# Kernel optimization log

Measured on AMD Instinct MI355X. Metric: run time of the kernel, lower is better.

Reference implementation:

```python
import jax, jax.numpy as jnp
import numpy as np

N_NODES = 100000
N_EDGES = 2000000
D_IN = 4
HID = 64


def setup_inputs() -> dict:
    key = jax.random.key(0)
    ks = jax.random.split(key, 8)
    node_feats = jax.random.normal(ks[0], (N_NODES, D_IN), dtype=jnp.float32)
    pairs = jax.random.randint(ks[1], (N_EDGES, 2), 0, N_NODES, dtype=jnp.int64)
    # Kaiming-ish init scaling
    W1 = jax.random.normal(ks[2], (D_IN, HID), dtype=jnp.float32) / np.sqrt(D_IN)
    b1 = jnp.zeros((HID,), dtype=jnp.float32)
    W2 = jax.random.normal(ks[3], (HID, HID), dtype=jnp.float32) / np.sqrt(HID)
    b2 = jnp.zeros((HID,), dtype=jnp.float32)
    We1 = jax.random.normal(ks[4], (3 * HID, HID), dtype=jnp.float32) / np.sqrt(3 * HID)
    be1 = jnp.zeros((HID,), dtype=jnp.float32)
    We2 = jax.random.normal(ks[5], (HID, 1), dtype=jnp.float32) / np.sqrt(HID)
    be2 = jnp.zeros((1,), dtype=jnp.float32)
    return {"node_feats": node_feats, "pairs": pairs, "W1": W1, "b1": b1,
            "W2": W2, "b2": b2, "We1": We1, "be1": be1, "We2": We2, "be2": be2}


def reference(node_feats, pairs, W1, b1, W2, b2, We1, be1, We2, be2):
    # node MLP: Linear -> ReLU -> Linear -> ReLU
    H = jax.nn.relu(node_feats @ W1 + b1)      # [N, HID]
    H = jax.nn.relu(H @ W2 + b2)               # [N, HID]
    # vectorized gather over all edge pairs (replaces Python loop)
    hu = H[pairs[:, 0]]                        # [E, HID]
    hv = H[pairs[:, 1]]                        # [E, HID]
    E = jnp.concatenate([hu, hv, jnp.abs(hu - hv)], axis=-1)  # [E, 3*HID]
    # edge MLP: Linear -> ReLU -> Linear, squeeze last dim
    scores = (jax.nn.relu(E @ We1 + be1) @ We2 + be2)[:, 0]   # [E]
    return scores
```

## Files before the change

kernel.cpp:

```cpp
#include <hip/hip_runtime.h>

#define N_NODES 100000
#define N_EDGES 2000000

typedef __bf16 bf16x8 __attribute__((ext_vector_type(8)));
typedef float f32x4 __attribute__((ext_vector_type(4)));
typedef float f32x16 __attribute__((ext_vector_type(16)));

#define AS1 __attribute__((address_space(1)))
#define AS3 __attribute__((address_space(3)))

__device__ __forceinline__ unsigned f2bf_rne(float f) {
  unsigned u = __builtin_bit_cast(unsigned, f);
  u += 0x7FFFu + ((u >> 16) & 1u);
  return u >> 16;
}

__device__ __forceinline__ unsigned pack_rhu(float lo, float hi) {
  unsigned ulo = __builtin_bit_cast(unsigned, lo) + 0x8000u;
  unsigned uhi = __builtin_bit_cast(unsigned, hi) + 0x8000u;
  return __builtin_amdgcn_perm(uhi, ulo, 0x07060302u);
}

__device__ __forceinline__ unsigned absdiff_pack(unsigned a, unsigned b) {
  float alo = __builtin_bit_cast(float, a << 16);
  float ahi = __builtin_bit_cast(float, a & 0xFFFF0000u);
  float blo = __builtin_bit_cast(float, b << 16);
  float bhi = __builtin_bit_cast(float, b & 0xFFFF0000u);
  return pack_rhu(fabsf(alo - blo), fabsf(ahi - bhi));
}

__global__ __launch_bounds__(64, 1) void node_mfma_kernel(
    const float* __restrict__ X, const float* __restrict__ W1,
    const float* __restrict__ b1, const float* __restrict__ W2,
    const float* __restrict__ b2, unsigned short* __restrict__ H) {
  const int lane = threadIdx.x;
  const int l15 = lane & 15;
  const int quad = lane >> 4;

  float w1v[2][4][8], b1v[2][8];
#pragma unroll
  for (int c = 0; c < 2; ++c)
#pragma unroll
    for (int j = 0; j < 8; ++j) {
      int col = c * 32 + quad * 8 + j;
      b1v[c][j] = b1[col];
#pragma unroll
      for (int d = 0; d < 4; ++d) w1v[c][d][j] = W1[d * 64 + col];
    }

  uint4 afr[2][4];
#pragma unroll
  for (int c = 0; c < 2; ++c)
#pragma unroll
    for (int mt = 0; mt < 4; ++mt) {
      unsigned w[4];
#pragma unroll
      for (int p = 0; p < 4; ++p) {
        int k = c * 32 + quad * 8 + 2 * p;
        unsigned lo = f2bf_rne(W2[k * 64 + mt * 16 + l15]);
        unsigned hi = f2bf_rne(W2[(k + 1) * 64 + mt * 16 + l15]);
        w[p] = lo | (hi << 16);
      }
      afr[c][mt] = make_uint4(w[0], w[1], w[2], w[3]);
    }
  float b2v[16];
#pragma unroll
  for (int mt = 0; mt < 4; ++mt)
#pragma unroll
    for (int r = 0; r < 4; ++r) b2v[mt * 4 + r] = b2[mt * 16 + quad * 4 + r];

  const int ntiles = N_NODES / 16;
  for (int tile = blockIdx.x; tile < ntiles; tile += gridDim.x) {
    float4 xv = ((const float4*)X)[tile * 16 + l15];

    uint4 bfr[2];
#pragma unroll
    for (int c = 0; c < 2; ++c) {
      unsigned w[4];
#pragma unroll
      for (int p = 0; p < 4; ++p) {
        float h0 = fmaxf(b1v[c][2 * p] + xv.x * w1v[c][0][2 * p] +
                             xv.y * w1v[c][1][2 * p] + xv.z * w1v[c][2][2 * p] +
                             xv.w * w1v[c][3][2 * p],
                         0.f);
        float h1 = fmaxf(b1v[c][2 * p + 1] + xv.x * w1v[c][0][2 * p + 1] +
                             xv.y * w1v[c][1][2 * p + 1] +
                             xv.z * w1v[c][2][2 * p + 1] +
                             xv.w * w1v[c][3][2 * p + 1],
                         0.f);
        w[p] = pack_rhu(h0, h1);
      }
      bfr[c] = make_uint4(w[0], w[1], w[2], w[3]);
    }

    f32x4 acc[4];
#pragma unroll
    for (int mt = 0; mt < 4; ++mt) acc[mt] = (f32x4){0.f, 0.f, 0.f, 0.f};
#pragma unroll
    for (int c = 0; c < 2; ++c)
#pragma unroll
      for (int mt = 0; mt < 4; ++mt)
        acc[mt] = __builtin_amdgcn_mfma_f32_16x16x32_bf16(
            __builtin_bit_cast(bf16x8, afr[c][mt]),
            __builtin_bit_cast(bf16x8, bfr[c]), acc[mt], 0, 0, 0);

    unsigned short* hrow = H + (tile * 16 + l15) * 64;
#pragma unroll
    for (int mt = 0; mt < 4; ++mt) {
      unsigned lo = pack_rhu(fmaxf(acc[mt][0] + b2v[mt * 4 + 0], 0.f),
                             fmaxf(acc[mt][1] + b2v[mt * 4 + 1], 0.f));
      unsigned hi = pack_rhu(fmaxf(acc[mt][2] + b2v[mt * 4 + 2], 0.f),
                             fmaxf(acc[mt][3] + b2v[mt * 4 + 3], 0.f));
      *(uint2*)(hrow + mt * 16 + quad * 4) = make_uint2(lo, hi);
    }
  }
}

__global__ __launch_bounds__(256, 2) void edge_mlp_kernel(
    const unsigned short* __restrict__ H, const int* __restrict__ pairs,
    const float* __restrict__ We1, const float* __restrict__ be1,
    const float* __restrict__ We2, const float* __restrict__ be2,
    float* __restrict__ out) {
  __shared__ uint4 wlds[26 * 64];
  __shared__ uint4 gbuf[4 * 512];
  const int tid = threadIdx.x;

  for (int s = tid; s < 26 * 64; s += 256) {
    int f = s >> 6, ln = s & 63;
    int c = f >> 1, mt = f & 1;
    int col = mt * 32 + (ln & 31);
    uint4 val;
    if (c < 12) {
      int kb = c * 16 + (ln >> 5) * 8;
      val.x = f2bf_rne(We1[(kb + 0) * 64 + col]) |
              (f2bf_rne(We1[(kb + 1) * 64 + col]) << 16);
      val.y = f2bf_rne(We1[(kb + 2) * 64 + col]) |
              (f2bf_rne(We1[(kb + 3) * 64 + col]) << 16);
      val.z = f2bf_rne(We1[(kb + 4) * 64 + col]) |
              (f2bf_rne(We1[(kb + 5) * 64 + col]) << 16);
      val.w = f2bf_rne(We1[(kb + 6) * 64 + col]) |
              (f2bf_rne(We1[(kb + 7) * 64 + col]) << 16);
    } else {
      val.x = ((ln >> 5) == 0) ? f2bf_rne(be1[col]) : 0u;
      val.y = 0u;
      val.z = 0u;
      val.w = 0u;
    }
    wlds[s] = val;
  }

  const int lane = tid & 63;
  const int n = lane & 31;
  const int half = lane >> 5;
  const int wave = tid >> 6;
  const int rowsel = lane >> 3;
  const int swzc = (lane & 7) ^ rowsel;

  uint4* gw = &gbuf[wave * 512];

  uint4 b13u = make_uint4((half == 0) ? 0x00003F80u : 0u, 0u, 0u, 0u);

  float we2v[32];
#pragma unroll
  for (int mt = 0; mt < 2; ++mt)
#pragma unroll
    for (int r = 0; r < 16; ++r)
      we2v[mt * 16 + r] = We2[mt * 32 + (r & 3) + 8 * (r >> 2) + 4 * half];
  const float be2v = be2[0];
  __syncthreads();

  const uint4* rb[4];
#pragma unroll
  for (int c = 0; c < 4; ++c) rb[c] = gw + n * 8 + (((2 * c + half) ^ (n & 7)));

  const int wid = blockIdx.x * 4 + wave;
  const int nw = gridDim.x * 4;
  const int ntiles = N_EDGES / 32;
  const int last = ntiles - 1;
  const int2* pairs2 = (const int2*)pairs;

  auto issue_gathers = [&](int2 pr0, int2 pr1, int2 pr2, int2 pr3) {
    int2 prs[4] = {pr0, pr1, pr2, pr3};
#pragma unroll
    for (int k = 0; k < 4; ++k) {
      const AS1 unsigned* gu =
          (const AS1 unsigned*)(H + (size_t)prs[k].x * 64) + swzc * 4;
      const AS1 unsigned* gv =
          (const AS1 unsigned*)(H + (size_t)prs[k].y * 64) + swzc * 4;
      __builtin_amdgcn_global_load_lds(gu, (AS3 unsigned*)(gw + k * 64), 16, 0,
                                       0);
      __builtin_amdgcn_global_load_lds(gv,
                                       (AS3 unsigned*)(gw + 256 + k * 64), 16,
                                       0, 0);
    }
  };

  int2 pr[4];
  {
    int t0 = wid;
#pragma unroll
    for (int k = 0; k < 4; ++k) pr[k] = pairs2[t0 * 32 + k * 8 + rowsel];
    issue_gathers(pr[0], pr[1], pr[2], pr[3]);
    int t1 = wid + nw <= last ? wid + nw : last;
#pragma unroll
    for (int k = 0; k < 4; ++k) pr[k] = pairs2[t1 * 32 + k * 8 + rowsel];
  }

  for (int tile = wid; tile < ntiles; tile += nw) {
    __builtin_amdgcn_s_waitcnt(0x0F70);
    __builtin_amdgcn_sched_barrier(0);

    uint4 hu[4], hv[4];
#pragma unroll
    for (int c = 0; c < 4; ++c) {
      hu[c] = rb[c][0];
      hv[c] = rb[c][256];
    }

    uint4 ab[4];
#pragma unroll
    for (int c = 0; c < 4; ++c) {
      ab[c].x = absdiff_pack(hu[c].x, hv[c].x);
      ab[c].y = absdiff_pack(hu[c].y, hv[c].y);
      ab[c].z = absdiff_pack(hu[c].z, hv[c].z);
      ab[c].w = absdiff_pack(hu[c].w, hv[c].w);
    }

    f32x16 acc[2];
    acc[0] = (f32x16)(0.f);
    acc[1] = (f32x16)(0.f);
    const uint4* wf = wlds + lane;
#pragma unroll
    for (int c = 0; c < 13; ++c) {
      uint4 bu = (c < 4) ? hu[c]
                         : (c < 8) ? hv[c - 4] : (c < 12 ? ab[c - 8] : b13u);
      bf16x8 b = __builtin_bit_cast(bf16x8, bu);
#pragma unroll
      for (int mt = 0; mt < 2; ++mt) {
        bf16x8 a = __builtin_bit_cast(bf16x8, wf[(c * 2 + mt) * 64]);
        acc[mt] =
            __builtin_amdgcn_mfma_f32_32x32x16_bf16(a, b, acc[mt], 0, 0, 0);
      }
    }

    __builtin_amdgcn_s_waitcnt(0xC07F);
    __builtin_amdgcn_sched_barrier(0);

    issue_gathers(pr[0], pr[1], pr[2], pr[3]);
    {
      int t2 = tile + 2 * nw <= last ? tile + 2 * nw : last;
#pragma unroll
      for (int k = 0; k < 4; ++k) pr[k] = pairs2[t2 * 32 + k * 8 + rowsel];
    }

    float s = 0.f;
#pragma unroll
    for (int mt = 0; mt < 2; ++mt)
#pragma unroll
      for (int r = 0; r < 16; ++r)
        s += fmaxf(acc[mt][r], 0.f) * we2v[mt * 16 + r];
    s += __shfl_xor(s, 32);
    if (half == 0) out[tile * 32 + n] = s + be2v;
  }
}

extern "C" void kernel_launch(void* const* d_in, const int* in_sizes, int n_in,
                              void* d_out, int out_size, void* d_ws,
                              size_t ws_size, hipStream_t stream) {
  const float* X = (const float*)d_in[0];
  const int* pairs = (const int*)d_in[1];
  const float* W1 = (const float*)d_in[2];
  const float* b1 = (const float*)d_in[3];
  const float* W2 = (const float*)d_in[4];
  const float* b2 = (const float*)d_in[5];
  const float* We1 = (const float*)d_in[6];
  const float* be1 = (const float*)d_in[7];
  const float* We2 = (const float*)d_in[8];
  const float* be2 = (const float*)d_in[9];
  float* out = (float*)d_out;
  unsigned short* H = (unsigned short*)d_ws;

  node_mfma_kernel<<<1024, 64, 0, stream>>>(X, W1, b1, W2, b2, H);
  edge_mlp_kernel<<<512, 256, 0, stream>>>(H, pairs, We1, be1, We2, be2, out);
}
```

Measured before the change: 164.4 us.

## Keep edge weights in registers and double-buffer gather LDS per wave

Moves the We1/be1 MFMA A-fragments from shared memory into registers (26 uint4 per lane) and removes the block-wide weight staging and __syncthreads. It also splits each wave's gather buffer into two halves, so the next tile's global_load_lds gathers are issued before the current tile's MFMAs rather than after, which overlaps gather latency with compute. The loop is unrolled by two with clamped tile indices, and a dummy scratch load is used to keep the vmcnt wait arithmetic consistent. The extra ~104 VGPRs for weights may reduce occupancy, and doubling the LDS per wave also raises pressure.

```diff
diff --git a/kernel.cpp b/kernel.cpp
--- a/kernel.cpp
+++ b/kernel.cpp
@@ -122,34 +122,9 @@
     const float* __restrict__ We1, const float* __restrict__ be1,
     const float* __restrict__ We2, const float* __restrict__ be2,
     float* __restrict__ out) {
-  __shared__ uint4 wlds[26 * 64];
-  __shared__ uint4 gbuf[4 * 512];
+  __shared__ uint4 gbuf[4][2][512];
+  __shared__ uint4 scratch[64];
   const int tid = threadIdx.x;
-
-  for (int s = tid; s < 26 * 64; s += 256) {
-    int f = s >> 6, ln = s & 63;
-    int c = f >> 1, mt = f & 1;
-    int col = mt * 32 + (ln & 31);
-    uint4 val;
-    if (c < 12) {
-      int kb = c * 16 + (ln >> 5) * 8;
-      val.x = f2bf_rne(We1[(kb + 0) * 64 + col]) |
-              (f2bf_rne(We1[(kb + 1) * 64 + col]) << 16);
-      val.y = f2bf_rne(We1[(kb + 2) * 64 + col]) |
-              (f2bf_rne(We1[(kb + 3) * 64 + col]) << 16);
-      val.z = f2bf_rne(We1[(kb + 4) * 64 + col]) |
-              (f2bf_rne(We1[(kb + 5) * 64 + col]) << 16);
-      val.w = f2bf_rne(We1[(kb + 6) * 64 + col]) |
-              (f2bf_rne(We1[(kb + 7) * 64 + col]) << 16);
-    } else {
-      val.x = ((ln >> 5) == 0) ? f2bf_rne(be1[col]) : 0u;
-      val.y = 0u;
-      val.z = 0u;
-      val.w = 0u;
-    }
-    wlds[s] = val;
-  }
-
   const int lane = tid & 63;
   const int n = lane & 31;
   const int half = lane >> 5;
@@ -157,9 +132,26 @@
   const int rowsel = lane >> 3;
   const int swzc = (lane & 7) ^ rowsel;
 
-  uint4* gw = &gbuf[wave * 512];
-
-  uint4 b13u = make_uint4((half == 0) ? 0x00003F80u : 0u, 0u, 0u, 0u);
+  uint4 afr[13][2];
+#pragma unroll
+  for (int c = 0; c < 12; ++c)
+#pragma unroll
+    for (int mt = 0; mt < 2; ++mt) {
+      int col = mt * 32 + n;
+      int kb = c * 16 + half * 8;
+      unsigned w[4];
+#pragma unroll
+      for (int p = 0; p < 4; ++p)
+        w[p] = f2bf_rne(We1[(kb + 2 * p) * 64 + col]) |
+               (f2bf_rne(We1[(kb + 2 * p + 1) * 64 + col]) << 16);
+      afr[c][mt] = make_uint4(w[0], w[1], w[2], w[3]);
+    }
+#pragma unroll
+  for (int mt = 0; mt < 2; ++mt)
+    afr[12][mt] =
+        make_uint4((half == 0) ? f2bf_rne(be1[mt * 32 + n]) : 0u, 0u, 0u, 0u);
+
+  const uint4 b13u = make_uint4((half == 0) ? 0x00003F80u : 0u, 0u, 0u, 0u);
 
   float we2v[32];
 #pragma unroll
@@ -168,11 +160,12 @@
     for (int r = 0; r < 16; ++r)
       we2v[mt * 16 + r] = We2[mt * 32 + (r & 3) + 8 * (r >> 2) + 4 * half];
   const float be2v = be2[0];
-  __syncthreads();
-
-  const uint4* rb[4];
-#pragma unroll
-  for (int c = 0; c < 4; ++c) rb[c] = gw + n * 8 + (((2 * c + half) ^ (n & 7)));
+
+  uint4* const bufA = &gbuf[wave][0][0];
+  uint4* const bufB = &gbuf[wave][1][0];
+  int rbo[4];
+#pragma unroll
+  for (int c = 0; c < 4; ++c) rbo[c] = n * 8 + ((2 * c + half) ^ (n & 7));
 
   const int wid = blockIdx.x * 4 + wave;
   const int nw = gridDim.x * 4;
@@ -180,44 +173,52 @@
   const int last = ntiles - 1;
   const int2* pairs2 = (const int2*)pairs;
 
-  auto issue_gathers = [&](int2 pr0, int2 pr1, int2 pr2, int2 pr3) {
-    int2 prs[4] = {pr0, pr1, pr2, pr3};
+  auto issue_gathers = [&](uint4* dst, const int2* prs) {
 #pragma unroll
     for (int k = 0; k < 4; ++k) {
       const AS1 unsigned* gu =
           (const AS1 unsigned*)(H + (size_t)prs[k].x * 64) + swzc * 4;
       const AS1 unsigned* gv =
           (const AS1 unsigned*)(H + (size_t)prs[k].y * 64) + swzc * 4;
-      __builtin_amdgcn_global_load_lds(gu, (AS3 unsigned*)(gw + k * 64), 16, 0,
-                                       0);
-      __builtin_amdgcn_global_load_lds(gv,
-                                       (AS3 unsigned*)(gw + 256 + k * 64), 16,
+      __builtin_amdgcn_global_load_lds(gu, (AS3 unsigned*)(dst + k * 64), 16,
                                        0, 0);
+      __builtin_amdgcn_global_load_lds(
+          gv, (AS3 unsigned*)(dst + 256 + k * 64), 16, 0, 0);
     }
   };
 
   int2 pr[4];
   {
-    int t0 = wid;
-#pragma unroll
-    for (int k = 0; k < 4; ++k) pr[k] = pairs2[t0 * 32 + k * 8 + rowsel];
-    issue_gathers(pr[0], pr[1], pr[2], pr[3]);
+#pragma unroll
+    for (int k = 0; k < 4; ++k) pr[k] = pairs2[wid * 32 + k * 8 + rowsel];
+    issue_gathers(bufA, pr);
     int t1 = wid + nw <= last ? wid + nw : last;
 #pragma unroll
     for (int k = 0; k < 4; ++k) pr[k] = pairs2[t1 * 32 + k * 8 + rowsel];
+    __builtin_amdgcn_global_load_lds((const AS1 unsigned*)H,
+                                     (AS3 unsigned*)scratch, 16, 0, 0);
   }
 
-  for (int tile = wid; tile < ntiles; tile += nw) {
-    __builtin_amdgcn_s_waitcnt(0x0F70);
+  auto body = [&](int tc, uint4* CONS, uint4* FILL) {
     __builtin_amdgcn_sched_barrier(0);
-
+    __builtin_amdgcn_s_waitcnt(0x0F75);
+    __builtin_amdgcn_sched_barrier(0);
+
+    issue_gathers(FILL, pr);
+    __builtin_amdgcn_sched_barrier(0);
+    {
+      int tn = tc + 2 * nw <= last ? tc + 2 * nw : last;
+#pragma unroll
+      for (int k = 0; k < 4; ++k) pr[k] = pairs2[tn * 32 + k * 8 + rowsel];
+    }
+
+    const int t = tc <= last ? tc : last;
     uint4 hu[4], hv[4];
 #pragma unroll
     for (int c = 0; c < 4; ++c) {
-      hu[c] = rb[c][0];
-      hv[c] = rb[c][256];
-    }
-
+      hu[c] = CONS[rbo[c]];
+      hv[c] = CONS[256 + rbo[c]];
+    }
     uint4 ab[4];
 #pragma unroll
     for (int c = 0; c < 4; ++c) {
@@ -230,28 +231,15 @@
     f32x16 acc[2];
     acc[0] = (f32x16)(0.f);
     acc[1] = (f32x16)(0.f);
-    const uint4* wf = wlds + lane;
 #pragma unroll
     for (int c = 0; c < 13; ++c) {
       uint4 bu = (c < 4) ? hu[c]
                          : (c < 8) ? hv[c - 4] : (c < 12 ? ab[c - 8] : b13u);
       bf16x8 b = __builtin_bit_cast(bf16x8, bu);
 #pragma unroll
-      for (int mt = 0; mt < 2; ++mt) {
-        bf16x8 a = __builtin_bit_cast(bf16x8, wf[(c * 2 + mt) * 64]);
-        acc[mt] =
-            __builtin_amdgcn_mfma_f32_32x32x16_bf16(a, b, acc[mt], 0, 0, 0);
-      }
-    }
-
-    __builtin_amdgcn_s_waitcnt(0xC07F);
-    __builtin_amdgcn_sched_barrier(0);
-
-    issue_gathers(pr[0], pr[1], pr[2], pr[3]);
-    {
-      int t2 = tile + 2 * nw <= last ? tile + 2 * nw : last;
-#pragma unroll
-      for (int k = 0; k < 4; ++k) pr[k] = pairs2[t2 * 32 + k * 8 + rowsel];
+      for (int mt = 0; mt < 2; ++mt)
+        acc[mt] = __builtin_amdgcn_mfma_f32_32x32x16_bf16(
+            __builtin_bit_cast(bf16x8, afr[c][mt]), b, acc[mt], 0, 0, 0);
     }
 
     float s = 0.f;
@@ -261,7 +249,12 @@
       for (int r = 0; r < 16; ++r)
         s += fmaxf(acc[mt][r], 0.f) * we2v[mt * 16 + r];
     s += __shfl_xor(s, 32);
-    if (half == 0) out[tile * 32 + n] = s + be2v;
+    if (half == 0) out[t * 32 + n] = s + be2v;
+  };
+
+  for (int t = wid; t < ntiles; t += 2 * nw) {
+    body(t, bufA, bufB);
+    body(t + nw, bufB, bufA);
   }
 }
 
```

Result: faster. 159.6 us (-3.0%).
